# Kernel tuning notes

Measured on AMD Instinct MI355X. Metric: run time of the kernel, lower is better.

## Reference

```python
import jax, jax.numpy as jnp
import numpy as np

B, N, P, C = 2, 1024, 32, 256   # batch, num queries, in_points, eff_in_dim(=in_dim, G=1)
OP = 32                          # out_points
HID = 128                        # parameter_generator hidden width
TOTAL = C * C + OP * P           # channel + spatial mixing params per query


def setup_inputs() -> dict:
    key = jax.random.key(0)
    ks = jax.random.split(key, 8)
    sc = lambda k, shape, s=0.02: jax.random.normal(k, shape, jnp.float32) * s
    return {
        "x": jax.random.normal(ks[0], (B, N, 1, P, C), jnp.float32),
        "query": jax.random.normal(ks[1], (B, N, C), jnp.float32),
        # LayerNorm initialized unit-norm style (gamma * width**-0.5), bias zero
        "ln_w": jnp.full((C,), C ** -0.5, jnp.float32),
        "ln_b": jnp.zeros((C,), jnp.float32),
        "w1": sc(ks[2], (HID, C)),
        "b1": jnp.zeros((HID,), jnp.float32),
        "w2": sc(ks[3], (TOTAL, HID)),
        "b2": sc(ks[4], (TOTAL,), 0.05),
        "m_beta": jnp.zeros((C,), jnp.float32),
        "s_beta": jnp.zeros((OP,), jnp.float32),
        "proj_w": sc(ks[5], (C, OP * C)),
        "proj_b": jnp.zeros((C,), jnp.float32),
    }


def reference(x, query, ln_w, ln_b, w1, b1, w2, b2, m_beta, s_beta, proj_w, proj_b):
    # parameter_generator: LayerNorm(eps=1e-6) -> Linear(C,128) -> Linear(128,TOTAL)
    mu = jnp.mean(query, axis=-1, keepdims=True)
    var = jnp.var(query, axis=-1, keepdims=True)  # biased, matches torch LayerNorm
    q = (query - mu) * jax.lax.rsqrt(var + 1e-6) * ln_w + ln_b
    h = q @ w1.T + b1                               # [B,N,128]
    params = h @ w2.T + b2                          # [B,N,TOTAL]

    cm = params[..., : C * C].reshape(B, N, C, C)   # channel mixing [B,N,Cin,Cout]
    sm = params[..., C * C :].reshape(B, N, OP, P)  # spatial mixing [B,N,OP,P]

    xs = x[:, :, 0]                                 # [B,N,P,C] (g==1)
    # baddbmm(channel_bias, x, channel_mixing) then GELU (exact erf)
    out = jnp.einsum('bnpc,bncd->bnpd', xs, cm) + m_beta
    out = jax.nn.gelu(out, approximate=False)
    # baddbmm(spatial_bias, spatial_mixing, out) then GELU
    out = jnp.einsum('bnop,bnpd->bnod', sm, out) + s_beta[None, None, :, None]
    out = jax.nn.gelu(out, approximate=False)

    out = out.reshape(B, N, OP * C) @ proj_w.T + proj_b  # tuo_proj -> [B,N,C]
    return out
```

## Files before the change

kernel.cpp:

```cpp
#include <hip/hip_runtime.h>
#include <hip/hip_bf16.h>

#define TKN   2048
#define CDIM  256
#define PDIM  32
#define ODIM  32
#define HIDD  128
#define CCSZ  65536
#define TOTSZ 66560
#define KSPL  16

typedef unsigned short u16;
typedef __bf16 bf16x8 __attribute__((ext_vector_type(8)));
typedef float f32x4 __attribute__((ext_vector_type(4)));
typedef unsigned short u16x4 __attribute__((ext_vector_type(4)));
typedef unsigned short u16x8 __attribute__((ext_vector_type(8)));

__device__ __forceinline__ u16 f2b(float f){
  __hip_bfloat16 h = __float2bfloat16(f);
  return *reinterpret_cast<u16*>(&h);
}
__device__ __forceinline__ float gelu_exact(float x){
  return 0.5f * x * (1.0f + erff(x * 0.70710678118654752f));
}

__global__ __launch_bounds__(256) void k_prep_h(
    const float* __restrict__ query, const float* __restrict__ ln_w,
    const float* __restrict__ ln_b, const float* __restrict__ w1,
    const float* __restrict__ b1, u16* __restrict__ H){
  const int t = blockIdx.x;
  const int tid = threadIdx.x;
  __shared__ float qs[CDIM];
  __shared__ float red[8];
  __shared__ float stat[2];
  float v = query[(size_t)t*CDIM + tid];
  float s = v, s2 = v*v;
  #pragma unroll
  for(int o=32;o>0;o>>=1){ s += __shfl_down(s,o,64); s2 += __shfl_down(s2,o,64); }
  const int wv = tid>>6;
  if((tid&63)==0){ red[wv]=s; red[4+wv]=s2; }
  __syncthreads();
  if(tid==0){
    float ss=red[0]+red[1]+red[2]+red[3];
    float qq=red[4]+red[5]+red[6]+red[7];
    float mu=ss/(float)CDIM;
    float var=qq/(float)CDIM - mu*mu;
    stat[0]=mu; stat[1]=rsqrtf(var+1e-6f);
  }
  __syncthreads();
  qs[tid] = (v - stat[0])*stat[1]*ln_w[tid] + ln_b[tid];
  __syncthreads();
  if(tid < HIDD){
    const float* wr = w1 + (size_t)tid*CDIM;
    float acc = b1[tid];
    #pragma unroll 8
    for(int c=0;c<CDIM;c++) acc += qs[c]*wr[c];
    H[(size_t)t*HIDD + tid] = f2b(acc);
  }
}

__global__ __launch_bounds__(256) void k_prep_w2(
    const float* __restrict__ w2, const float* __restrict__ b2,
    u16* __restrict__ w2s, float* __restrict__ b2p){
  const int gid = blockIdx.x*256 + threadIdx.x;
  const int n  = gid >> 4;
  const int ch = gid & 15;
  if(n >= TOTSZ) return;
  int j;
  if(n < CCSZ){
    const int f = n >> 9, rem = n & 511;
    const int g = rem >> 7, r = (rem >> 3) & 15, e = rem & 7;
    const int d = (f >> 3)*16 + r;
    const int c = (f & 7)*32 + g*8 + e;
    j = c*256 + d;
  } else {
    j = n;
  }
  const float* src = w2 + (size_t)j*HIDD + ch*8;
  u16x8 tv;
  #pragma unroll
  for(int i=0;i<8;i++) tv[i] = f2b(src[i]);
  const int q = n >> 7, ks = ch >> 2, nt8 = (n >> 4) & 7, kg = ch & 3, r15 = n & 15;
  *(u16x8*)(w2s + ((size_t)((q*4 + ks)*8 + nt8))*512 + (kg*16 + r15)*8) = tv;
  if(ch == 0) b2p[n] = b2[j];
}

__global__ __launch_bounds__(256) void k_prep_pw(
    const float* __restrict__ pw, u16* __restrict__ pwb){
  const int gid = blockIdx.x*256 + threadIdx.x;
  const float* s = pw + (size_t)gid*8;
  u16x8 tv;
  #pragma unroll
  for(int i=0;i<8;i++) tv[i] = f2b(s[i]);
  *(u16x8*)(pwb + (size_t)gid*8) = tv;
}

__global__ __launch_bounds__(256, 3) void k_params(
    const u16* __restrict__ H, const u16* __restrict__ w2s,
    const float* __restrict__ b2p, u16* __restrict__ pbuf, int chnk){
  __shared__ __align__(16) u16 S[4][16][136];
  const int tid = threadIdx.x;
  const int lane = tid & 63;
  const int w = tid >> 6;
  const int q = blockIdx.x;
  const int n0 = q * 128;
  const int r15 = lane & 15, g = lane >> 4;
  const int tb = blockIdx.y*128 + w*16;
  bf16x8 afr[2][4];
  #pragma unroll
  for(int m=0;m<2;m++){
    const u16* ap = H + (size_t)(tb + m*64 + r15)*HIDD + g*8;
    #pragma unroll
    for(int ks=0;ks<4;ks++) afr[m][ks] = *(const bf16x8*)(ap + ks*32);
  }
  float b2v[8];
  #pragma unroll
  for(int nt=0;nt<8;nt++) b2v[nt] = b2p[n0 + nt*16 + r15];
  f32x4 acc[2][8] = {};
  #pragma unroll
  for(int ks=0;ks<4;ks++){
    bf16x8 bfr[8];
    #pragma unroll
    for(int nt=0;nt<8;nt++)
      bfr[nt] = *(const bf16x8*)(w2s + ((size_t)((q*4 + ks)*8 + nt))*512 + lane*8);
    #pragma unroll
    for(int m=0;m<2;m++)
      #pragma unroll
      for(int nt=0;nt<8;nt++)
        acc[m][nt] = __builtin_amdgcn_mfma_f32_16x16x32_bf16(afr[m][ks], bfr[nt], acc[m][nt], 0,0,0);
  }
  #pragma unroll
  for(int m=0;m<2;m++){
    #pragma unroll
    for(int nt=0;nt<8;nt++)
      #pragma unroll
      for(int r=0;r<4;r++)
        S[w][g*4 + r][nt*16 + r15] = f2b(acc[m][nt][r] + b2v[nt]);
    u16* dst = pbuf + ((size_t)q*chnk + tb + m*64)*128;
    #pragma unroll
    for(int i=0;i<4;i++){
      const int lt = i*4 + (lane >> 4);
      const int jc = lane & 15;
      *(u16x8*)(dst + (size_t)lt*128 + jc*8) = *(const u16x8*)&S[w][lt][jc*8];
    }
  }
}

__global__ __launch_bounds__(512, 4) void k_token(
    const float* __restrict__ xg, const u16* __restrict__ pbuf,
    const float* __restrict__ m_beta, const float* __restrict__ s_beta,
    u16* __restrict__ out2, int chnk){
  __shared__ u16 xs[PDIM][264];
  __shared__ u16 smt[ODIM][40];
  __shared__ u16 o1[CDIM][40];
  const int tl = blockIdx.x;
  const int tid = threadIdx.x;
  const int lane = tid & 63;
  const int w = tid >> 6;
  const int r15 = lane & 15, g = lane >> 4;

  bf16x8 af[2][8];
  #pragma unroll
  for(int ks=0;ks<8;ks++)
    #pragma unroll
    for(int mt=0;mt<2;mt++){
      const int f = (w*2+mt)*8 + ks;
      af[mt][ks] = *(const bf16x8*)(pbuf + ((size_t)(4*f + g)*chnk + tl)*128 + r15*8);
    }

  {
    const f32x4* src = (const f32x4*)(xg + (size_t)tl*8192);
    #pragma unroll
    for(int i=0;i<4;i++){
      const int idx = tid + 512*i;
      f32x4 v = src[idx];
      const int flat = idx*4;
      const int p = flat >> 8, c = flat & 255;
      u16x4 t4; t4[0]=f2b(v[0]); t4[1]=f2b(v[1]); t4[2]=f2b(v[2]); t4[3]=f2b(v[3]);
      *(u16x4*)&xs[p][c] = t4;
    }
  }
  if(tid < 128){
    const u16* s = pbuf + ((size_t)(512 + (tid>>4))*chnk + tl)*128 + (tid&15)*8;
    const int o = (tid*8) >> 5, p = (tid*8) & 31;
    *(u16x8*)&smt[o][p] = *(const u16x8*)s;
  }
  __syncthreads();

  f32x4 acc[2][2] = {};
  #pragma unroll
  for(int ks=0;ks<8;ks++){
    bf16x8 bf[2];
    #pragma unroll
    for(int nt=0;nt<2;nt++){
      const int p = nt*16 + r15;
      bf[nt] = *(const bf16x8*)&xs[p][ks*32 + g*8];
    }
    #pragma unroll
    for(int mt=0;mt<2;mt++)
      #pragma unroll
      for(int nt=0;nt<2;nt++)
        acc[mt][nt] = __builtin_amdgcn_mfma_f32_16x16x32_bf16(af[mt][ks], bf[nt], acc[mt][nt], 0,0,0);
  }
  #pragma unroll
  for(int mt=0;mt<2;mt++){
    const int d0 = w*32 + mt*16 + g*4;
    const f32x4 mb = *(const f32x4*)&m_beta[d0];
    #pragma unroll
    for(int nt=0;nt<2;nt++){
      const int p = nt*16 + r15;
      #pragma unroll
      for(int r=0;r<4;r++)
        o1[d0+r][p] = f2b(gelu_exact(acc[mt][nt][r] + mb[r]));
    }
  }
  __syncthreads();

  f32x4 acc2[2][2] = {};
  {
    bf16x8 af2[2], bf2[2];
    #pragma unroll
    for(int mt=0;mt<2;mt++){
      const int d = w*32 + mt*16 + r15;
      af2[mt] = *(const bf16x8*)&o1[d][g*8];
    }
    #pragma unroll
    for(int nt=0;nt<2;nt++){
      const int o = nt*16 + r15;
      bf2[nt] = *(const bf16x8*)&smt[o][g*8];
    }
    #pragma unroll
    for(int mt=0;mt<2;mt++)
      #pragma unroll
      for(int nt=0;nt<2;nt++)
        acc2[mt][nt] = __builtin_amdgcn_mfma_f32_16x16x32_bf16(af2[mt], bf2[nt], acc2[mt][nt], 0,0,0);
  }
  u16 (*o2t)[264] = xs;
  #pragma unroll
  for(int nt=0;nt<2;nt++){
    const int o = nt*16 + r15;
    const float sb = s_beta[o];
    #pragma unroll
    for(int mt=0;mt<2;mt++){
      const int d0 = w*32 + mt*16 + g*4;
      u16x4 t4;
      #pragma unroll
      for(int r=0;r<4;r++) t4[r] = f2b(gelu_exact(acc2[mt][nt][r] + sb));
      *(u16x4*)&o2t[o][d0] = t4;
    }
  }
  __syncthreads();
  {
    u16* dst = out2 + (size_t)tl*8192;
    #pragma unroll
    for(int i=0;i<2;i++){
      const int flat = (i*512 + tid)*8;
      const int o = flat >> 8, dd = flat & 255;
      *(u16x8*)(dst + flat) = *(const u16x8*)&o2t[o][dd];
    }
  }
}

__global__ __launch_bounds__(512) void k_proj(
    const u16* __restrict__ out2, const u16* __restrict__ pwb,
    float* __restrict__ part){
  __shared__ u16 Ab[2][64*32];
  __shared__ u16 Bb[2][256*32];
  const int tid = threadIdx.x;
  const int lane = tid & 63, w = tid >> 6;
  const int r15 = lane & 15, g = lane >> 4;
  const int m0 = blockIdx.x * 64;
  const int k0 = blockIdx.y * 512;
  const int wm = (w >> 2) * 32;
  const int wn = (w & 3) * 64;
  const int srow = lane >> 2;
  const int cs   = lane & 3;
  const int a_row = (w & 3)*16 + srow;
  const u16* a_src = out2 + (size_t)(m0 + a_row)*8192 + k0 + (size_t)((cs ^ (a_row & 3))*8);
  const int b_row0 = (2*w)*16 + srow;
  const int b_row1 = (2*w+1)*16 + srow;
  const u16* b_src0 = pwb + (size_t)b_row0*8192 + k0 + (size_t)((cs ^ (b_row0 & 3))*8);
  const u16* b_src1 = pwb + (size_t)b_row1*8192 + k0 + (size_t)((cs ^ (b_row1 & 3))*8);

  f32x4 acc[2][4] = {};

  #define GL16(gp, lp) __builtin_amdgcn_global_load_lds( \
      (const __attribute__((address_space(1))) unsigned int*)(gp), \
      (__attribute__((address_space(3))) unsigned int*)(lp), 16, 0, 0)
  #define STAGE(buf, kt) do{                                         \
    const int ko = (kt)*32;                                          \
    if(w < 4) GL16(a_src + ko, (char*)&Ab[buf][0] + w*1024);         \
    GL16(b_src0 + ko, (char*)&Bb[buf][0] + (2*w)*1024);              \
    GL16(b_src1 + ko, (char*)&Bb[buf][0] + (2*w+1)*1024);            \
  }while(0)

  STAGE(0, 0);
  __syncthreads();
  int cur = 0;
  for(int kt=0; kt<16; kt++){
    if(kt < 15){ STAGE(cur^1, kt+1); }
    bf16x8 af[2], bf[4];
    #pragma unroll
    for(int mt=0;mt<2;mt++){
      const int row = wm + mt*16 + r15;
      af[mt] = *(const bf16x8*)((char*)&Ab[cur][0] + row*64 + ((g ^ (row&3))*16));
    }
    #pragma unroll
    for(int nt=0;nt<4;nt++){
      const int row = wn + nt*16 + r15;
      bf[nt] = *(const bf16x8*)((char*)&Bb[cur][0] + row*64 + ((g ^ (row&3))*16));
    }
    #pragma unroll
    for(int mt=0;mt<2;mt++)
      #pragma unroll
      for(int nt=0;nt<4;nt++)
        acc[mt][nt] = __builtin_amdgcn_mfma_f32_16x16x32_bf16(af[mt], bf[nt], acc[mt][nt], 0,0,0);
    __syncthreads();
    cur ^= 1;
  }
  #undef STAGE
  #undef GL16

  float* pbase = part + (size_t)blockIdx.y*TKN*CDIM;
  #pragma unroll
  for(int mt=0;mt<2;mt++)
    #pragma unroll
    for(int nt=0;nt<4;nt++){
      const int t = m0 + wm + mt*16 + g*4;
      const int e = wn + nt*16 + r15;
      #pragma unroll
      for(int r=0;r<4;r++)
        pbase[(size_t)(t+r)*CDIM + e] = acc[mt][nt][r];
    }
}

__global__ __launch_bounds__(256) void k_combine(
    const float* __restrict__ part, const float* __restrict__ pb,
    float* __restrict__ out){
  const int i4 = blockIdx.x*256 + threadIdx.x;
  const int e4 = (i4 & 63)*4;
  f32x4 s = *(const f32x4*)&pb[e4];
  #pragma unroll
  for(int z=0;z<KSPL;z++) s += *(const f32x4*)&part[(size_t)z*524288 + (size_t)i4*4];
  *(f32x4*)&out[(size_t)i4*4] = s;
}

extern "C" void kernel_launch(void* const* d_in, const int* in_sizes, int n_in,
                              void* d_out, int out_size, void* d_ws, size_t ws_size,
                              hipStream_t stream){
  const float* x     = (const float*)d_in[0];
  const float* query = (const float*)d_in[1];
  const float* ln_w  = (const float*)d_in[2];
  const float* ln_b  = (const float*)d_in[3];
  const float* w1    = (const float*)d_in[4];
  const float* b1    = (const float*)d_in[5];
  const float* w2    = (const float*)d_in[6];
  const float* b2    = (const float*)d_in[7];
  const float* m_beta= (const float*)d_in[8];
  const float* s_beta= (const float*)d_in[9];
  const float* pw    = (const float*)d_in[10];
  const float* pb    = (const float*)d_in[11];
  float* out = (float*)d_out;
  char* ws = (char*)d_ws;

  const size_t need_big = 192u*1024u*1024u;
  const int chnk = (ws_size >= need_big) ? 1024 : 256;
  const int nch  = TKN / chnk;

  size_t off = 0;
  u16* H     = (u16*)(ws + off);  off += (size_t)TKN*HIDD*2;
  u16* w2s   = (u16*)(ws + off);  off += (size_t)TOTSZ*HIDD*2;
  float* b2p = (float*)(ws + off);off += (size_t)TOTSZ*4;
  u16* pwb   = (u16*)(ws + off);  off += (size_t)CDIM*8192*2;
  u16* pbuf  = (u16*)(ws + off);  off += (size_t)chnk*TOTSZ*2;
  u16* out2  = (u16*)(ws + off);  off += (size_t)TKN*8192*2;
  float* part= (float*)pbuf;

  k_prep_h<<<TKN, 256, 0, stream>>>(query, ln_w, ln_b, w1, b1, H);
  k_prep_w2<<<4160, 256, 0, stream>>>(w2, b2, w2s, b2p);
  k_prep_pw<<<1024, 256, 0, stream>>>(pw, pwb);
  for(int ch=0; ch<nch; ch++){
    k_params<<<dim3(520, chnk/128), 256, 0, stream>>>(H + (size_t)ch*chnk*HIDD, w2s, b2p, pbuf, chnk);
    k_token<<<chnk, 512, 0, stream>>>(x + (size_t)ch*chnk*8192, pbuf, m_beta, s_beta,
                                      out2 + (size_t)ch*chnk*8192, chnk);
  }
  k_proj<<<dim3(32,KSPL), 512, 0, stream>>>(out2, pwb, part);
  k_combine<<<512, 256, 0, stream>>>(part, pb, out);
}
```

Baseline: 228.2 us.

## Pre-convert x to swizzled bf16 and emit token outputs in MFMA fragment order

Adds a prep kernel that converts x to bf16 in an XOR-swizzled layout, so k_token can stage it into LDS with direct global-to-LDS loads instead of converting fp32 in-kernel. Spatial-mixing weights now go straight into registers instead of through LDS. The second-stage output is written in fragment order without a transposing LDS pass, and proj_w is permuted in prep to match. One barrier and some LDS traffic are dropped, at the cost of an extra pass over x, more workspace (which can push chunking to the smaller size), and a lower occupancy hint on k_token.

```diff
diff --git a/kernel.cpp b/kernel.cpp
--- a/kernel.cpp
+++ b/kernel.cpp
@@ -23,6 +23,11 @@
 __device__ __forceinline__ float gelu_exact(float x){
   return 0.5f * x * (1.0f + erff(x * 0.70710678118654752f));
 }
+__device__ __forceinline__ void gload16(const void* g, void* l){
+  __builtin_amdgcn_global_load_lds(
+      (const __attribute__((address_space(1))) unsigned int*)g,
+      (__attribute__((address_space(3))) unsigned int*)l, 16, 0, 0);
+}
 
 __global__ __launch_bounds__(256) void k_prep_h(
     const float* __restrict__ query, const float* __restrict__ ln_w,
@@ -56,6 +61,26 @@
     #pragma unroll 8
     for(int c=0;c<CDIM;c++) acc += qs[c]*wr[c];
     H[(size_t)t*HIDD + tid] = f2b(acc);
+  }
+}
+
+__global__ __launch_bounds__(256) void k_prep_x(
+    const float* __restrict__ x, u16* __restrict__ xb){
+  const int t = blockIdx.x;
+  const int tid = threadIdx.x;
+  const float* src = x + (size_t)t*8192;
+  u16* dst = xb + (size_t)t*8192;
+  #pragma unroll
+  for(int i=0;i<4;i++){
+    const int flat = (i*256+tid)*8;
+    const int p = flat >> 8, c = flat & 255;
+    const int cc = (c >> 3) ^ (p & 15);
+    f32x4 v0 = *(const f32x4*)(src + flat);
+    f32x4 v1 = *(const f32x4*)(src + flat + 4);
+    u16x8 o;
+    o[0]=f2b(v0[0]); o[1]=f2b(v0[1]); o[2]=f2b(v0[2]); o[3]=f2b(v0[3]);
+    o[4]=f2b(v1[0]); o[5]=f2b(v1[1]); o[6]=f2b(v1[2]); o[7]=f2b(v1[3]);
+    *(u16x8*)(dst + p*256 + cc*8) = o;
   }
 }
 
@@ -88,11 +113,18 @@
 __global__ __launch_bounds__(256) void k_prep_pw(
     const float* __restrict__ pw, u16* __restrict__ pwb){
   const int gid = blockIdx.x*256 + threadIdx.x;
-  const float* s = pw + (size_t)gid*8;
-  u16x8 tv;
-  #pragma unroll
-  for(int i=0;i<8;i++) tv[i] = f2b(s[i]);
-  *(u16x8*)(pwb + (size_t)gid*8) = tv;
+  const int e = gid >> 11;
+  const int kp = (gid & 2047)*4;
+  const int grp = kp >> 8;
+  const int rem = kp & 255;
+  const int g = rem >> 6, r15 = (rem >> 2) & 15;
+  const int w_ = grp >> 2, mt = (grp >> 1) & 1, nt = grp & 1;
+  const int o = nt*16 + r15;
+  const int d0 = w_*32 + mt*16 + g*4;
+  const float* s = pw + (size_t)e*8192 + o*256 + d0;
+  u16x4 tv;
+  tv[0]=f2b(s[0]); tv[1]=f2b(s[1]); tv[2]=f2b(s[2]); tv[3]=f2b(s[3]);
+  *(u16x4*)(pwb + (size_t)e*8192 + kp) = tv;
 }
 
 __global__ __launch_bounds__(256, 3) void k_params(
@@ -146,13 +178,12 @@
   }
 }
 
-__global__ __launch_bounds__(512, 4) void k_token(
-    const float* __restrict__ xg, const u16* __restrict__ pbuf,
+__global__ __launch_bounds__(512, 2) void k_token(
+    const u16* __restrict__ xb, const u16* __restrict__ pbuf,
     const float* __restrict__ m_beta, const float* __restrict__ s_beta,
     u16* __restrict__ out2, int chnk){
-  __shared__ u16 xs[PDIM][264];
-  __shared__ u16 smt[ODIM][40];
-  __shared__ u16 o1[CDIM][40];
+  __shared__ u16 xs[PDIM*256];
+  __shared__ u16 o1[CDIM][36];
   const int tl = blockIdx.x;
   const int tid = threadIdx.x;
   const int lane = tid & 63;
@@ -167,23 +198,17 @@
       const int f = (w*2+mt)*8 + ks;
       af[mt][ks] = *(const bf16x8*)(pbuf + ((size_t)(4*f + g)*chnk + tl)*128 + r15*8);
     }
-
+  bf16x8 bf2[2];
+  #pragma unroll
+  for(int nt=0;nt<2;nt++){
+    const int o = nt*16 + r15;
+    bf2[nt] = *(const bf16x8*)(pbuf + ((size_t)(512 + (o>>2))*chnk + tl)*128 + (o&3)*32 + g*8);
+  }
   {
-    const f32x4* src = (const f32x4*)(xg + (size_t)tl*8192);
-    #pragma unroll
-    for(int i=0;i<4;i++){
-      const int idx = tid + 512*i;
-      f32x4 v = src[idx];
-      const int flat = idx*4;
-      const int p = flat >> 8, c = flat & 255;
-      u16x4 t4; t4[0]=f2b(v[0]); t4[1]=f2b(v[1]); t4[2]=f2b(v[2]); t4[3]=f2b(v[3]);
-      *(u16x4*)&xs[p][c] = t4;
-    }
-  }
-  if(tid < 128){
-    const u16* s = pbuf + ((size_t)(512 + (tid>>4))*chnk + tl)*128 + (tid&15)*8;
-    const int o = (tid*8) >> 5, p = (tid*8) & 31;
-    *(u16x8*)&smt[o][p] = *(const u16x8*)s;
+    const u16* src = xb + (size_t)tl*8192;
+    #pragma unroll
+    for(int i=0;i<2;i++)
+      gload16(src + (i*512 + w*64 + lane)*8, (char*)xs + (i*8+w)*1024);
   }
   __syncthreads();
 
@@ -194,7 +219,7 @@
     #pragma unroll
     for(int nt=0;nt<2;nt++){
       const int p = nt*16 + r15;
-      bf[nt] = *(const bf16x8*)&xs[p][ks*32 + g*8];
+      bf[nt] = *(const bf16x8*)&xs[p*256 + (((ks*4+g) ^ r15)<<3)];
     }
     #pragma unroll
     for(int mt=0;mt<2;mt++)
@@ -214,49 +239,30 @@
         o1[d0+r][p] = f2b(gelu_exact(acc[mt][nt][r] + mb[r]));
     }
   }
-  __syncthreads();
-
   f32x4 acc2[2][2] = {};
   {
-    bf16x8 af2[2], bf2[2];
+    bf16x8 af2[2];
     #pragma unroll
     for(int mt=0;mt<2;mt++){
       const int d = w*32 + mt*16 + r15;
       af2[mt] = *(const bf16x8*)&o1[d][g*8];
     }
     #pragma unroll
-    for(int nt=0;nt<2;nt++){
-      const int o = nt*16 + r15;
-      bf2[nt] = *(const bf16x8*)&smt[o][g*8];
-    }
-    #pragma unroll
     for(int mt=0;mt<2;mt++)
       #pragma unroll
       for(int nt=0;nt<2;nt++)
         acc2[mt][nt] = __builtin_amdgcn_mfma_f32_16x16x32_bf16(af2[mt], bf2[nt], acc2[mt][nt], 0,0,0);
   }
-  u16 (*o2t)[264] = xs;
+  u16* dst = out2 + (size_t)tl*8192 + w*1024;
   #pragma unroll
   for(int nt=0;nt<2;nt++){
-    const int o = nt*16 + r15;
-    const float sb = s_beta[o];
+    const float sb = s_beta[nt*16 + r15];
     #pragma unroll
     for(int mt=0;mt<2;mt++){
-      const int d0 = w*32 + mt*16 + g*4;
       u16x4 t4;
       #pragma unroll
       for(int r=0;r<4;r++) t4[r] = f2b(gelu_exact(acc2[mt][nt][r] + sb));
-      *(u16x4*)&o2t[o][d0] = t4;
-    }
-  }
-  __syncthreads();
-  {
-    u16* dst = out2 + (size_t)tl*8192;
-    #pragma unroll
-    for(int i=0;i<2;i++){
-      const int flat = (i*512 + tid)*8;
-      const int o = flat >> 8, dd = flat & 255;
-      *(u16x8*)(dst + flat) = *(const u16x8*)&o2t[o][dd];
+      *(u16x4*)(dst + (mt*2+nt)*256 + lane*4) = t4;
     }
   }
 }
@@ -284,14 +290,11 @@
 
   f32x4 acc[2][4] = {};
 
-  #define GL16(gp, lp) __builtin_amdgcn_global_load_lds( \
-      (const __attribute__((address_space(1))) unsigned int*)(gp), \
-      (__attribute__((address_space(3))) unsigned int*)(lp), 16, 0, 0)
   #define STAGE(buf, kt) do{                                         \
     const int ko = (kt)*32;                                          \
-    if(w < 4) GL16(a_src + ko, (char*)&Ab[buf][0] + w*1024);         \
-    GL16(b_src0 + ko, (char*)&Bb[buf][0] + (2*w)*1024);              \
-    GL16(b_src1 + ko, (char*)&Bb[buf][0] + (2*w+1)*1024);            \
+    if(w < 4) gload16(a_src + ko, (char*)&Ab[buf][0] + w*1024);      \
+    gload16(b_src0 + ko, (char*)&Bb[buf][0] + (2*w)*1024);           \
+    gload16(b_src1 + ko, (char*)&Bb[buf][0] + (2*w+1)*1024);         \
   }while(0)
 
   STAGE(0, 0);
@@ -319,7 +322,6 @@
     cur ^= 1;
   }
   #undef STAGE
-  #undef GL16
 
   float* pbase = part + (size_t)blockIdx.y*TKN*CDIM;
   #pragma unroll
@@ -363,7 +365,7 @@
   float* out = (float*)d_out;
   char* ws = (char*)d_ws;
 
-  const size_t need_big = 192u*1024u*1024u;
+  const size_t need_big = 230u*1024u*1024u;
   const int chnk = (ws_size >= need_big) ? 1024 : 256;
   const int nch  = TKN / chnk;
 
@@ -372,16 +374,18 @@
   u16* w2s   = (u16*)(ws + off);  off += (size_t)TOTSZ*HIDD*2;
   float* b2p = (float*)(ws + off);off += (size_t)TOTSZ*4;
   u16* pwb   = (u16*)(ws + off);  off += (size_t)CDIM*8192*2;
+  u16* xb    = (u16*)(ws + off);  off += (size_t)TKN*8192*2;
   u16* pbuf  = (u16*)(ws + off);  off += (size_t)chnk*TOTSZ*2;
   u16* out2  = (u16*)(ws + off);  off += (size_t)TKN*8192*2;
   float* part= (float*)pbuf;
 
   k_prep_h<<<TKN, 256, 0, stream>>>(query, ln_w, ln_b, w1, b1, H);
+  k_prep_x<<<TKN, 256, 0, stream>>>(x, xb);
   k_prep_w2<<<4160, 256, 0, stream>>>(w2, b2, w2s, b2p);
-  k_prep_pw<<<1024, 256, 0, stream>>>(pw, pwb);
+  k_prep_pw<<<2048, 256, 0, stream>>>(pw, pwb);
   for(int ch=0; ch<nch; ch++){
     k_params<<<dim3(520, chnk/128), 256, 0, stream>>>(H + (size_t)ch*chnk*HIDD, w2s, b2p, pbuf, chnk);
-    k_token<<<chnk, 512, 0, stream>>>(x + (size_t)ch*chnk*8192, pbuf, m_beta, s_beta,
+    k_token<<<chnk, 512, 0, stream>>>(xb + (size_t)ch*chnk*8192, pbuf, m_beta, s_beta,
                                       out2 + (size_t)ch*chnk*8192, chnk);
   }
   k_proj<<<dim3(32,KSPL), 512, 0, stream>>>(out2, pwb, part);
```

New measurement: 251.7 us. 10.3% more time.
